# Kernel optimization log

Measured on AMD Instinct MI355X. Metric: run time of the kernel, lower is better.

## Reference

```python
import jax, jax.numpy as jnp
import numpy as np
from jax import lax

# SLAYER neuron / simulation constants (from netParams)
THETA = 10.0       # spike threshold
TAU_SR = 10.0      # synaptic (PSP) time constant
TAU_REF = 1.0      # refractory time constant
SCALE_REF = 2.0    # refractory scale
TAU_RHO = 1.0      # surrogate-gradient width (unused in fwd)
K_PSP = 32         # truncation length of SRM alpha kernel
K_REF = 16         # truncation length of refractory kernel

_t = np.arange(K_PSP, dtype=np.float64)
PSP_KERN = jnp.asarray((_t / TAU_SR) * np.exp(1.0 - _t / TAU_SR), jnp.float32)  # [K_PSP]
_tr = np.arange(1, K_REF + 1, dtype=np.float64)
REF_KERN = jnp.asarray(-SCALE_REF * THETA * (_tr / TAU_REF) * np.exp(1.0 - _tr / TAU_REF), jnp.float32)  # [K_REF]


def psp(x):
    """Causal temporal FIR filter with SRM alpha kernel; x: [..., T]."""
    sh = x.shape
    T = sh[-1]
    flat = x.reshape(-1, 1, T)                       # [B*, 1, T]
    k = PSP_KERN[::-1][None, None, :]                # correlation kernel (reversed)
    y = lax.conv_general_dilated(flat, k, (1,), [(K_PSP - 1, 0)])
    return y.reshape(sh)


def spike(u):
    """Threshold with refractory feedback, sequential over time. u: [..., T]."""
    uT = jnp.moveaxis(u, -1, 0)                      # [T, ...]
    buf0 = jnp.zeros(u.shape[:-1] + (K_REF,), u.dtype)

    def step(buf, ut):
        v = ut + buf[..., 0]
        s = (v >= THETA).astype(u.dtype)
        buf = jnp.concatenate([buf[..., 1:], jnp.zeros_like(buf[..., :1])], -1)
        buf = buf + s[..., None] * REF_KERN
        return buf, s

    _, sT = lax.scan(step, buf0, uT)
    return jnp.moveaxis(sT, 0, -1)


def conv_t(x, w, stride, pad):
    """2D conv applied independently per timestep. x: [N,C,H,W,T], w: [Co,C,kh,kw]."""
    N, C, H, W, T = x.shape
    xt = jnp.moveaxis(x, -1, 1).reshape(N * T, C, H, W)
    y = lax.conv_general_dilated(xt, w, (stride, stride), [(pad, pad), (pad, pad)])
    Co, Ho, Wo = y.shape[1], y.shape[2], y.shape[3]
    return jnp.moveaxis(y.reshape(N, T, Co, Ho, Wo), 1, -1)


def pool_t(x):
    """SLAYER sum-pool 2x2/s2 with weight 1.1*theta/kernel_area. x: [N,C,H,W,T]."""
    s = lax.reduce_window(x, np.float32(0.0), lax.add, (1, 1, 2, 2, 1), (1, 1, 2, 2, 1), 'VALID')
    return s * np.float32(1.1 * THETA / 4.0)


def setup_inputs() -> dict:
    key = jax.random.key(0)
    ks = jax.random.split(key, 5)
    spikeInput = (jax.random.uniform(ks[0], (4, 2, 256, 256, 50)) < 0.02).astype(jnp.float32)
    w1 = jax.random.normal(ks[1], (8, 2, 5, 5), jnp.float32) * 2.0
    w2 = jax.random.normal(ks[2], (16, 8, 3, 3), jnp.float32) * 1.5
    w3 = jax.random.normal(ks[3], (32, 16, 3, 3), jnp.float32) * 1.5
    w_fc = jax.random.normal(ks[4], (2, 32, 8, 8), jnp.float32) * 0.3
    return {"spikeInput": spikeInput, "w1": w1, "w2": w2, "w3": w3, "w_fc": w_fc}


def reference(spikeInput, w1, w2, w3, w_fc):
    x = spike(conv_t(psp(spikeInput), w1, 2, 1))   # [4,8,127,127,50]
    x = spike(pool_t(psp(x)))                      # [4,8,63,63,50]
    x = spike(conv_t(psp(x), w2, 2, 1))            # [4,16,32,32,50]
    x = spike(pool_t(psp(x)))                      # [4,16,16,16,50]
    x = spike(conv_t(psp(x), w3, 2, 1))            # [4,32,8,8,50]
    u = psp(x)
    out = jnp.einsum('ochw,nchwt->not', w_fc, u)   # dense over (C,H,W)
    return spike(out[:, :, None, None, :])         # [4,2,1,1,50]
```

## Files before the change

### kernel.cpp

```cpp
#include <hip/hip_runtime.h>
#include <cmath>

struct K32 { float k[32]; };
struct K16 { float k[16]; };

#define THETA 10.0f

__global__ __launch_bounds__(128)
void psp_kernel(const float* __restrict__ in, float* __restrict__ out,
                int nrows, K32 pk) {
  __shared__ __align__(16) float lds[64 * 50];
  const int rowBase = blockIdx.x * 64;
  const int tid = threadIdx.x;
  const int vr = min(64, nrows - rowBase);
  const int n4 = (vr * 50) >> 2;
  const float4* g4 = (const float4*)(in + (size_t)rowBase * 50);
  for (int i = tid; i < n4; i += 128) *(float4*)(&lds[4 * i]) = g4[i];
  __syncthreads();
  const int r = tid & 63;
  const int part = tid >> 6;
  const bool act = r < vr;
  float x[50];
  if (act) {
    if (part == 0) {
#pragma unroll
      for (int t = 0; t < 32; ++t) x[t] = lds[r * 50 + t];
    } else {
#pragma unroll
      for (int t = 0; t < 50; ++t) x[t] = lds[r * 50 + t];
    }
  }
  __syncthreads();
  if (act) {
    if (part == 0) {
#pragma unroll
      for (int t = 0; t < 32; ++t) {
        float a = 0.f;
#pragma unroll
        for (int k = 31; k >= 0; --k)
          if (t - k >= 0) a += x[t - k] * pk.k[k];
        lds[r * 50 + t] = a;
      }
    } else {
#pragma unroll
      for (int t = 32; t < 50; ++t) {
        float a = 0.f;
#pragma unroll
        for (int k = 31; k >= 0; --k)
          a += x[t - k] * pk.k[k];
        lds[r * 50 + t] = a;
      }
    }
  }
  __syncthreads();
  float4* o4 = (float4*)(out + (size_t)rowBase * 50);
  for (int i = tid; i < n4; i += 128) o4[i] = *(const float4*)(&lds[4 * i]);
}

template <int CIN, int COUT, int KK, int HIN, int WIN, int S1H, int S1W,
          int S2H, int S2W>
__global__ __launch_bounds__(256)
void conv_pps_kernel(const float* __restrict__ x, const float* __restrict__ w,
                     float* __restrict__ s2out, K32 pk, K16 rk) {
  constexpr int WT = 4;
  constexpr int SW = 8;
  constexpr int XR = 2 * (WT - 1) + KK;
  constexpr int GROUPS = (S1W + SW - 1) / SW;
  constexpr int NROW = COUT * 2 * SW;
  __shared__ float lds[NROW * 51];
  const int tid = threadIdx.x;
  const int wave = tid >> 6;
  const int lane = tid & 63;
  const int group = blockIdx.x % GROUPS;
  const int rest = blockIdx.x / GROUPS;
  const int hop = rest % S2H;
  const int n = rest / S2H;
  const int ho_off = wave & 1;
  const int wo_half = wave >> 1;
  const int ho = 2 * hop + ho_off;
  const int wo0 = group * SW + wo_half * WT;
  const int tt = lane < 50 ? lane : 49;

  float acc[COUT][WT] = {};
  for (int c = 0; c < CIN; ++c) {
#pragma unroll
    for (int kh = 0; kh < KK; ++kh) {
      const int hi = 2 * ho + kh - 1;
      if ((unsigned)hi >= (unsigned)HIN) continue;
      float xr[XR];
#pragma unroll
      for (int i = 0; i < XR; ++i) {
        const int wi = 2 * wo0 - 1 + i;
        xr[i] = ((unsigned)wi < (unsigned)WIN)
                    ? x[(((size_t)(n * CIN + c) * HIN + hi) * WIN + wi) * 50 + tt]
                    : 0.f;
      }
#pragma unroll
      for (int co = 0; co < COUT; ++co)
#pragma unroll
        for (int kw = 0; kw < KK; ++kw) {
          const float wv = w[((co * CIN + c) * KK + kh) * KK + kw];
#pragma unroll
          for (int wl = 0; wl < WT; ++wl)
            acc[co][wl] += xr[2 * wl + kw] * wv;
        }
    }
  }
  if (lane < 50) {
#pragma unroll
    for (int co = 0; co < COUT; ++co)
#pragma unroll
      for (int wl = 0; wl < WT; ++wl)
        lds[((co * 2 + ho_off) * SW + wo_half * WT + wl) * 51 + lane] = acc[co][wl];
  }
  __syncthreads();
  {
    const int r = tid & (NROW - 1);
    const int part = tid >> 7;
    const int wol = r & (SW - 1);
    const bool act = (group * SW + wol) < S1W;
    float xs[50];
    if (act) {
      if (part == 0) {
#pragma unroll
        for (int t = 0; t < 32; ++t) xs[t] = lds[r * 51 + t];
      } else {
#pragma unroll
        for (int t = 0; t < 50; ++t) xs[t] = lds[r * 51 + t];
      }
    }
    __syncthreads();
    if (act) {
      if (part == 0) {
        float buf[16];
#pragma unroll
        for (int j = 0; j < 16; ++j) buf[j] = 0.f;
#pragma unroll
        for (int t = 0; t < 32; ++t) {
          float v = xs[t] + buf[t & 15];
          buf[t & 15] = 0.f;
          float sp = 0.f;
          if (v >= THETA) {
            sp = 1.f;
#pragma unroll
            for (int j = 0; j < 16; ++j) buf[(t + 1 + j) & 15] += rk.k[j];
          }
          xs[t] = sp;
        }
#pragma unroll
        for (int t = 0; t < 32; ++t) {
          float a = 0.f;
#pragma unroll
          for (int k = 31; k >= 0; --k)
            if (t - k >= 0) a += xs[t - k] * pk.k[k];
          lds[r * 51 + t] = a;
        }
      } else {
        float buf[16];
#pragma unroll
        for (int j = 0; j < 16; ++j) buf[j] = 0.f;
#pragma unroll
        for (int t = 0; t < 50; ++t) {
          float v = xs[t] + buf[t & 15];
          buf[t & 15] = 0.f;
          float sp = 0.f;
          if (v >= THETA) {
            sp = 1.f;
#pragma unroll
            for (int j = 0; j < 16; ++j) buf[(t + 1 + j) & 15] += rk.k[j];
          }
          xs[t] = sp;
        }
#pragma unroll
        for (int t = 32; t < 50; ++t) {
          float a = 0.f;
#pragma unroll
          for (int k = 31; k >= 0; --k)
            a += xs[t - k] * pk.k[k];
          lds[r * 51 + t] = a;
        }
      }
    }
  }
  __syncthreads();
  if (tid < COUT * (SW / 2)) {
    const int co = tid / (SW / 2);
    const int wpl = tid % (SW / 2);
    const int wop = group * (SW / 2) + wpl;
    if (wop < S2W) {
      const int r00 = (co * 16 + 2 * wpl) * 51;
      const int r01 = (co * 16 + 2 * wpl + 1) * 51;
      const int r10 = (co * 16 + 8 + 2 * wpl) * 51;
      const int r11 = (co * 16 + 8 + 2 * wpl + 1) * 51;
      float* orow = s2out + (((size_t)(n * COUT + co) * S2H + hop) * S2W + wop) * 50;
      float buf[16];
#pragma unroll
      for (int j = 0; j < 16; ++j) buf[j] = 0.f;
      float prev = 0.f;
#pragma unroll
      for (int t = 0; t < 50; ++t) {
        const float u0 = (((lds[r00 + t] + lds[r01 + t]) + lds[r10 + t]) + lds[r11 + t]) * 2.75f;
        float v = u0 + buf[t & 15];
        buf[t & 15] = 0.f;
        float sp = 0.f;
        if (v >= THETA) {
          sp = 1.f;
#pragma unroll
          for (int j = 0; j < 16; ++j) buf[(t + 1 + j) & 15] += rk.k[j];
        }
        if (t & 1) *(float2*)(orow + t - 1) = make_float2(prev, sp);
        else prev = sp;
      }
    }
  }
}

template <int CIN, int COUT, int KK, int WT, int HIN, int WIN, int HOUT, int WOUT>
__global__ __launch_bounds__(256)
void conv_fir_spike_kernel(const float* __restrict__ x, const float* __restrict__ w,
                           float* __restrict__ s, K32 pk, K16 rk) {
  constexpr int XR = 2 * (WT - 1) + KK;
  constexpr int TW = 4 * WT;
  constexpr int GROUPS = (WOUT + TW - 1) / TW;
  constexpr int NROW = COUT * TW;
  __shared__ float lds[NROW * 51];
  const int tid = threadIdx.x;
  const int wave = tid >> 6;
  const int lane = tid & 63;
  const int group = blockIdx.x % GROUPS;
  const int rest = blockIdx.x / GROUPS;
  const int ho = rest % HOUT;
  const int n = rest / HOUT;
  const int wo0 = group * TW + wave * WT;
  const int tt = lane < 50 ? lane : 49;

  float acc[COUT][WT] = {};
  for (int c = 0; c < CIN; ++c) {
#pragma unroll
    for (int kh = 0; kh < KK; ++kh) {
      const int hi = 2 * ho + kh - 1;
      if ((unsigned)hi >= (unsigned)HIN) continue;
      float xr[XR];
#pragma unroll
      for (int i = 0; i < XR; ++i) {
        const int wi = 2 * wo0 - 1 + i;
        xr[i] = ((unsigned)wi < (unsigned)WIN)
                    ? x[(((size_t)(n * CIN + c) * HIN + hi) * WIN + wi) * 50 + tt]
                    : 0.f;
      }
#pragma unroll
      for (int co = 0; co < COUT; ++co)
#pragma unroll
        for (int kw = 0; kw < KK; ++kw) {
          const float wv = w[((co * CIN + c) * KK + kh) * KK + kw];
#pragma unroll
          for (int wl = 0; wl < WT; ++wl)
            acc[co][wl] += xr[2 * wl + kw] * wv;
        }
    }
  }

  if (lane < 50) {
#pragma unroll
    for (int co = 0; co < COUT; ++co)
#pragma unroll
      for (int wl = 0; wl < WT; ++wl)
        lds[(co * TW + wave * WT + wl) * 51 + lane] = acc[co][wl];
  }
  __syncthreads();
  {
    const int r = tid % NROW;
    const int part = tid / NROW;
    const int wol = r % TW;
    const bool act = (part < 2) && (group * TW + wol < WOUT);
    float xs[50];
    if (act) {
      if (part == 0) {
#pragma unroll
        for (int t = 0; t < 25; ++t) xs[t] = lds[r * 51 + t];
      } else {
#pragma unroll
        for (int t = 0; t < 50; ++t) xs[t] = lds[r * 51 + t];
      }
    }
    __syncthreads();
    if (act) {
      if (part == 0) {
#pragma unroll
        for (int t = 0; t < 25; ++t) {
          float a = 0.f;
#pragma unroll
          for (int k = 31; k >= 0; --k)
            if (t - k >= 0) a += xs[t - k] * pk.k[k];
          lds[r * 51 + t] = a;
        }
      } else {
#pragma unroll
        for (int t = 25; t < 50; ++t) {
          float a = 0.f;
#pragma unroll
          for (int k = 31; k >= 0; --k)
            if (t - k >= 0) a += xs[t - k] * pk.k[k];
          lds[r * 51 + t] = a;
        }
      }
    }
  }
  __syncthreads();
  if (tid < NROW) {
    const int co = tid / TW;
    const int wol = tid - co * TW;
    const int wo = group * TW + wol;
    if (wo < WOUT) {
      float* orow = s + (((size_t)(n * COUT + co) * HOUT + ho) * WOUT + wo) * 50;
      float buf[16];
#pragma unroll
      for (int j = 0; j < 16; ++j) buf[j] = 0.f;
      float prev = 0.f;
#pragma unroll
      for (int t = 0; t < 50; ++t) {
        float v = lds[tid * 51 + t] + buf[t & 15];
        buf[t & 15] = 0.f;
        float sp = 0.f;
        if (v >= THETA) {
          sp = 1.f;
#pragma unroll
          for (int j = 0; j < 16; ++j) buf[(t + 1 + j) & 15] += rk.k[j];
        }
        if (t & 1) *(float2*)(orow + t - 1) = make_float2(prev, sp);
        else prev = sp;
      }
    }
  }
}

__global__ __launch_bounds__(128)
void pool_fir_spike_kernel(const float* __restrict__ in, float* __restrict__ out,
                           int Hin, int Win, int Hout, int Wout, K32 pk, K16 rk) {
  __shared__ __align__(16) float lds[64 * 50 + 16 * 50];
  const int tid = threadIdx.x;
  const int ho = blockIdx.x % Hout;
  const int nc = blockIdx.x / Hout;
  const float* b0 = in + ((size_t)(nc * Hin + 2 * ho) * Win) * 50;
  const int n4 = (2 * Win * 50) >> 2;
  const float4* g4 = (const float4*)b0;
  for (int i = tid; i < n4; i += 128) *(float4*)(&lds[4 * i]) = g4[i];
  __syncthreads();
  {
    const int r = tid & 15;
    const int part = tid >> 4;
    const bool act = (part < 2) && (r < Wout);
    const int c00 = (2 * r) * 50, c01 = c00 + 50;
    const int c10 = Win * 50 + c00, c11 = Win * 50 + c01;
    const int ro = 64 * 50 + r * 50;
    float xs[50];
    if (act) {
      if (part == 0) {
#pragma unroll
        for (int t = 0; t < 25; ++t)
          xs[t] = (((lds[c00 + t] + lds[c01 + t]) + lds[c10 + t]) + lds[c11 + t]) * 2.75f;
#pragma unroll
        for (int t = 0; t < 25; ++t) {
          float a = 0.f;
#pragma unroll
          for (int k = 31; k >= 0; --k)
            if (t - k >= 0) a += xs[t - k] * pk.k[k];
          lds[ro + t] = a;
        }
      } else {
#pragma unroll
        for (int t = 0; t < 50; ++t)
          xs[t] = (((lds[c00 + t] + lds[c01 + t]) + lds[c10 + t]) + lds[c11 + t]) * 2.75f;
#pragma unroll
        for (int t = 25; t < 50; ++t) {
          float a = 0.f;
#pragma unroll
          for (int k = 31; k >= 0; --k)
            if (t - k >= 0) a += xs[t - k] * pk.k[k];
          lds[ro + t] = a;
        }
      }
    }
  }
  __syncthreads();
  if (tid < 16 && tid < Wout) {
    const int ro = 64 * 50 + tid * 50;
    float* orow = out + (((size_t)nc * Hout + ho) * Wout + tid) * 50;
    float buf[16];
#pragma unroll
    for (int j = 0; j < 16; ++j) buf[j] = 0.f;
    float prev = 0.f;
#pragma unroll
    for (int t = 0; t < 50; ++t) {
      float v = lds[ro + t] + buf[t & 15];
      buf[t & 15] = 0.f;
      float sp = 0.f;
      if (v >= THETA) {
        sp = 1.f;
#pragma unroll
        for (int j = 0; j < 16; ++j) buf[(t + 1 + j) & 15] += rk.k[j];
      }
      if (t & 1) *(float2*)(orow + t - 1) = make_float2(prev, sp);
      else prev = sp;
    }
  }
}

__global__ __launch_bounds__(512)
void fc_fir_spike_kernel(const float* __restrict__ w, const float* __restrict__ s,
                         float* __restrict__ out, K32 pk, K16 rk) {
  __shared__ float lds[8 * 51];
  const int tid = threadIdx.x;
  const int wave = tid >> 6, lane = tid & 63;
  const int o = wave & 1, n = wave >> 1;
  const int tt = lane < 50 ? lane : 49;
  const float* wrow = w + (size_t)o * 2048;
  const float* ub = s + (size_t)n * 2048 * 50;
  float acc = 0.f;
#pragma unroll 32
  for (int i = 0; i < 2048; ++i) acc += wrow[i] * ub[(size_t)i * 50 + tt];
  if (lane < 50) lds[wave * 51 + lane] = acc;
  __syncthreads();
  {
    const int r = tid & 7;
    const int part = tid >> 3;
    const bool act = part < 2;
    float xs[50];
    if (act) {
      if (part == 0) {
#pragma unroll
        for (int t = 0; t < 25; ++t) xs[t] = lds[r * 51 + t];
      } else {
#pragma unroll
        for (int t = 0; t < 50; ++t) xs[t] = lds[r * 51 + t];
      }
    }
    __syncthreads();
    if (act) {
      if (part == 0) {
#pragma unroll
        for (int t = 0; t < 25; ++t) {
          float a = 0.f;
#pragma unroll
          for (int k = 31; k >= 0; --k)
            if (t - k >= 0) a += xs[t - k] * pk.k[k];
          lds[r * 51 + t] = a;
        }
      } else {
#pragma unroll
        for (int t = 25; t < 50; ++t) {
          float a = 0.f;
#pragma unroll
          for (int k = 31; k >= 0; --k)
            if (t - k >= 0) a += xs[t - k] * pk.k[k];
          lds[r * 51 + t] = a;
        }
      }
    }
  }
  __syncthreads();
  if (tid < 8) {
    float buf[16];
#pragma unroll
    for (int j = 0; j < 16; ++j) buf[j] = 0.f;
#pragma unroll
    for (int t = 0; t < 50; ++t) {
      float v = lds[tid * 51 + t] + buf[t & 15];
      buf[t & 15] = 0.f;
      float sp = 0.f;
      if (v >= THETA) {
        sp = 1.f;
#pragma unroll
        for (int j = 0; j < 16; ++j) buf[(t + 1 + j) & 15] += rk.k[j];
      }
      out[tid * 50 + t] = sp;
    }
  }
}

extern "C" void kernel_launch(void* const* d_in, const int* in_sizes, int n_in,
                              void* d_out, int out_size, void* d_ws, size_t ws_size,
                              hipStream_t stream) {
  const float* xin = (const float*)d_in[0];
  const float* w1  = (const float*)d_in[1];
  const float* w2  = (const float*)d_in[2];
  const float* w3  = (const float*)d_in[3];
  const float* wfc = (const float*)d_in[4];
  float* out = (float*)d_out;

  float* R0 = (float*)d_ws;
  float* R1 = R0 + 26214400;

  K32 pk;
  for (int k = 0; k < 32; ++k)
    pk.k[k] = (float)(((double)k / 10.0) * exp(1.0 - (double)k / 10.0));
  K16 rk;
  for (int j = 0; j < 16; ++j) {
    const double tr = (double)(j + 1);
    rk.k[j] = (float)(-2.0 * 10.0 * tr * exp(1.0 - tr));
  }

  psp_kernel<<<8192, 128, 0, stream>>>(xin, R0, 524288, pk);
  conv_pps_kernel<2, 8, 5, 256, 256, 127, 127, 63, 63>
      <<<4 * 63 * 16, 256, 0, stream>>>(R0, w1, R1, pk, rk);
  conv_fir_spike_kernel<8, 16, 3, 1, 63, 63, 32, 32>
      <<<4 * 32 * 8, 256, 0, stream>>>(R1, w2, R0, pk, rk);
  pool_fir_spike_kernel<<<4 * 16 * 16, 128, 0, stream>>>(R0, R1, 32, 32, 16, 16, pk, rk);
  conv_fir_spike_kernel<16, 32, 3, 1, 16, 16, 8, 8>
      <<<4 * 8 * 2, 256, 0, stream>>>(R1, w3, R0, pk, rk);
  fc_fir_spike_kernel<<<1, 512, 0, stream>>>(wfc, R0, out, pk, rk);
}
```

Before: 482.7 us.

## Fuse second conv stage with pool, PSP and spike into one kernel

Adds a kernel that computes conv2 for a 2x4 output tile, applies PSP filtering and refractory spiking in LDS, then does 2x2 sum-pooling, a second PSP and a second spike before writing the pooled output. This replaces the separate conv_fir_spike and pool_fir_spike launches. It removes one launch and the global write and read of the unpooled spike tensor. In exchange each block carries more serial work and there are fewer blocks, which may hurt latency hiding.

```diff
diff --git a/kernel.cpp b/kernel.cpp
--- a/kernel.cpp
+++ b/kernel.cpp
@@ -215,6 +215,187 @@
   }
 }
 
+template <int CIN, int COUT, int KK, int SW, int WT, int HIN, int WIN,
+          int S1H, int S1W, int S2H, int S2W>
+__global__ __launch_bounds__(256)
+void conv_pps2_kernel(const float* __restrict__ x, const float* __restrict__ w,
+                      float* __restrict__ s2out, K32 pk, K16 rk) {
+  constexpr int XR = 2 * (WT - 1) + KK;
+  constexpr int GROUPS = (S1W + SW - 1) / SW;
+  constexpr int NROW = COUT * 2 * SW;
+  constexpr int NROWP = COUT * (SW / 2);
+  __shared__ float lds[NROW * 51];
+  const int tid = threadIdx.x;
+  const int wave = tid >> 6;
+  const int lane = tid & 63;
+  const int group = blockIdx.x % GROUPS;
+  const int rest = blockIdx.x / GROUPS;
+  const int hop = rest % S2H;
+  const int n = rest / S2H;
+  const int ho_off = wave & 1;
+  const int wo_half = wave >> 1;
+  const int ho = 2 * hop + ho_off;
+  const int wo0 = group * SW + wo_half * WT;
+  const int tt = lane < 50 ? lane : 49;
+
+  float acc[COUT][WT] = {};
+  for (int c = 0; c < CIN; ++c) {
+#pragma unroll
+    for (int kh = 0; kh < KK; ++kh) {
+      const int hi = 2 * ho + kh - 1;
+      if ((unsigned)hi >= (unsigned)HIN) continue;
+      float xr[XR];
+#pragma unroll
+      for (int i = 0; i < XR; ++i) {
+        const int wi = 2 * wo0 - 1 + i;
+        xr[i] = ((unsigned)wi < (unsigned)WIN)
+                    ? x[(((size_t)(n * CIN + c) * HIN + hi) * WIN + wi) * 50 + tt]
+                    : 0.f;
+      }
+#pragma unroll
+      for (int co = 0; co < COUT; ++co)
+#pragma unroll
+        for (int kw = 0; kw < KK; ++kw) {
+          const float wv = w[((co * CIN + c) * KK + kh) * KK + kw];
+#pragma unroll
+          for (int wl = 0; wl < WT; ++wl)
+            acc[co][wl] += xr[2 * wl + kw] * wv;
+        }
+    }
+  }
+  if (lane < 50) {
+#pragma unroll
+    for (int co = 0; co < COUT; ++co)
+#pragma unroll
+      for (int wl = 0; wl < WT; ++wl)
+        lds[((co * 2 + ho_off) * SW + wo_half * WT + wl) * 51 + lane] = acc[co][wl];
+  }
+  __syncthreads();
+  {
+    const int r = tid & (NROW - 1);
+    const int part = tid >> 7;
+    float xs[50];
+    if (part == 0) {
+#pragma unroll
+      for (int t = 0; t < 32; ++t) xs[t] = lds[r * 51 + t];
+    } else {
+#pragma unroll
+      for (int t = 0; t < 50; ++t) xs[t] = lds[r * 51 + t];
+    }
+    __syncthreads();
+    if (part == 0) {
+#pragma unroll
+      for (int t = 0; t < 32; ++t) {
+        float a = 0.f;
+#pragma unroll
+        for (int k = 31; k >= 0; --k)
+          if (t - k >= 0) a += xs[t - k] * pk.k[k];
+        lds[r * 51 + t] = a;
+      }
+    } else {
+#pragma unroll
+      for (int t = 32; t < 50; ++t) {
+        float a = 0.f;
+#pragma unroll
+        for (int k = 31; k >= 0; --k)
+          a += xs[t - k] * pk.k[k];
+        lds[r * 51 + t] = a;
+      }
+    }
+  }
+  __syncthreads();
+  if (tid < NROW) {
+    float buf[16];
+#pragma unroll
+    for (int j = 0; j < 16; ++j) buf[j] = 0.f;
+#pragma unroll
+    for (int t = 0; t < 50; ++t) {
+      float v = lds[tid * 51 + t] + buf[t & 15];
+      buf[t & 15] = 0.f;
+      float sp = 0.f;
+      if (v >= THETA) {
+        sp = 1.f;
+#pragma unroll
+        for (int j = 0; j < 16; ++j) buf[(t + 1 + j) & 15] += rk.k[j];
+      }
+      lds[tid * 51 + t] = sp;
+    }
+  }
+  __syncthreads();
+  {
+    const int r = tid & (NROWP - 1);
+    const int part = tid >> 5;
+    const bool act = part < 2;
+    const int co = r / (SW / 2);
+    const int wpl = r % (SW / 2);
+    const int r00 = ((co * 2) * SW + 2 * wpl) * 51;
+    const int r01 = r00 + 51;
+    const int r10 = ((co * 2 + 1) * SW + 2 * wpl) * 51;
+    const int r11 = r10 + 51;
+    float xs[50];
+    if (act) {
+      if (part == 0) {
+#pragma unroll
+        for (int t = 0; t < 32; ++t)
+          xs[t] = (((lds[r00 + t] + lds[r01 + t]) + lds[r10 + t]) + lds[r11 + t]) * 2.75f;
+      } else {
+#pragma unroll
+        for (int t = 0; t < 50; ++t)
+          xs[t] = (((lds[r00 + t] + lds[r01 + t]) + lds[r10 + t]) + lds[r11 + t]) * 2.75f;
+      }
+    }
+    __syncthreads();
+    if (act) {
+      if (part == 0) {
+#pragma unroll
+        for (int t = 0; t < 32; ++t) {
+          float a = 0.f;
+#pragma unroll
+          for (int k = 31; k >= 0; --k)
+            if (t - k >= 0) a += xs[t - k] * pk.k[k];
+          lds[r00 + t] = a;
+        }
+      } else {
+#pragma unroll
+        for (int t = 32; t < 50; ++t) {
+          float a = 0.f;
+#pragma unroll
+          for (int k = 31; k >= 0; --k)
+            a += xs[t - k] * pk.k[k];
+          lds[r00 + t] = a;
+        }
+      }
+    }
+  }
+  __syncthreads();
+  if (tid < NROWP) {
+    const int co = tid / (SW / 2);
+    const int wpl = tid % (SW / 2);
+    const int wop = group * (SW / 2) + wpl;
+    if (wop < S2W) {
+      const int r00 = ((co * 2) * SW + 2 * wpl) * 51;
+      float* orow = s2out + (((size_t)(n * COUT + co) * S2H + hop) * S2W + wop) * 50;
+      float buf[16];
+#pragma unroll
+      for (int j = 0; j < 16; ++j) buf[j] = 0.f;
+      float prev = 0.f;
+#pragma unroll
+      for (int t = 0; t < 50; ++t) {
+        float v = lds[r00 + t] + buf[t & 15];
+        buf[t & 15] = 0.f;
+        float sp = 0.f;
+        if (v >= THETA) {
+          sp = 1.f;
+#pragma unroll
+          for (int j = 0; j < 16; ++j) buf[(t + 1 + j) & 15] += rk.k[j];
+        }
+        if (t & 1) *(float2*)(orow + t - 1) = make_float2(prev, sp);
+        else prev = sp;
+      }
+    }
+  }
+}
+
 template <int CIN, int COUT, int KK, int WT, int HIN, int WIN, int HOUT, int WOUT>
 __global__ __launch_bounds__(256)
 void conv_fir_spike_kernel(const float* __restrict__ x, const float* __restrict__ w,
@@ -334,78 +515,6 @@
   }
 }
 
-__global__ __launch_bounds__(128)
-void pool_fir_spike_kernel(const float* __restrict__ in, float* __restrict__ out,
-                           int Hin, int Win, int Hout, int Wout, K32 pk, K16 rk) {
-  __shared__ __align__(16) float lds[64 * 50 + 16 * 50];
-  const int tid = threadIdx.x;
-  const int ho = blockIdx.x % Hout;
-  const int nc = blockIdx.x / Hout;
-  const float* b0 = in + ((size_t)(nc * Hin + 2 * ho) * Win) * 50;
-  const int n4 = (2 * Win * 50) >> 2;
-  const float4* g4 = (const float4*)b0;
-  for (int i = tid; i < n4; i += 128) *(float4*)(&lds[4 * i]) = g4[i];
-  __syncthreads();
-  {
-    const int r = tid & 15;
-    const int part = tid >> 4;
-    const bool act = (part < 2) && (r < Wout);
-    const int c00 = (2 * r) * 50, c01 = c00 + 50;
-    const int c10 = Win * 50 + c00, c11 = Win * 50 + c01;
-    const int ro = 64 * 50 + r * 50;
-    float xs[50];
-    if (act) {
-      if (part == 0) {
-#pragma unroll
-        for (int t = 0; t < 25; ++t)
-          xs[t] = (((lds[c00 + t] + lds[c01 + t]) + lds[c10 + t]) + lds[c11 + t]) * 2.75f;
-#pragma unroll
-        for (int t = 0; t < 25; ++t) {
-          float a = 0.f;
-#pragma unroll
-          for (int k = 31; k >= 0; --k)
-            if (t - k >= 0) a += xs[t - k] * pk.k[k];
-          lds[ro + t] = a;
-        }
-      } else {
-#pragma unroll
-        for (int t = 0; t < 50; ++t)
-          xs[t] = (((lds[c00 + t] + lds[c01 + t]) + lds[c10 + t]) + lds[c11 + t]) * 2.75f;
-#pragma unroll
-        for (int t = 25; t < 50; ++t) {
-          float a = 0.f;
-#pragma unroll
-          for (int k = 31; k >= 0; --k)
-            if (t - k >= 0) a += xs[t - k] * pk.k[k];
-          lds[ro + t] = a;
-        }
-      }
-    }
-  }
-  __syncthreads();
-  if (tid < 16 && tid < Wout) {
-    const int ro = 64 * 50 + tid * 50;
-    float* orow = out + (((size_t)nc * Hout + ho) * Wout + tid) * 50;
-    float buf[16];
-#pragma unroll
-    for (int j = 0; j < 16; ++j) buf[j] = 0.f;
-    float prev = 0.f;
-#pragma unroll
-    for (int t = 0; t < 50; ++t) {
-      float v = lds[ro + t] + buf[t & 15];
-      buf[t & 15] = 0.f;
-      float sp = 0.f;
-      if (v >= THETA) {
-        sp = 1.f;
-#pragma unroll
-        for (int j = 0; j < 16; ++j) buf[(t + 1 + j) & 15] += rk.k[j];
-      }
-      if (t & 1) *(float2*)(orow + t - 1) = make_float2(prev, sp);
-      else prev = sp;
-    }
-  }
-}
-
 __global__ __launch_bounds__(512)
 void fc_fir_spike_kernel(const float* __restrict__ w, const float* __restrict__ s,
                          float* __restrict__ out, K32 pk, K16 rk) {
@@ -503,10 +612,9 @@
   psp_kernel<<<8192, 128, 0, stream>>>(xin, R0, 524288, pk);
   conv_pps_kernel<2, 8, 5, 256, 256, 127, 127, 63, 63>
       <<<4 * 63 * 16, 256, 0, stream>>>(R0, w1, R1, pk, rk);
-  conv_fir_spike_kernel<8, 16, 3, 1, 63, 63, 32, 32>
-      <<<4 * 32 * 8, 256, 0, stream>>>(R1, w2, R0, pk, rk);
-  pool_fir_spike_kernel<<<4 * 16 * 16, 128, 0, stream>>>(R0, R1, 32, 32, 16, 16, pk, rk);
+  conv_pps2_kernel<8, 16, 3, 4, 2, 63, 63, 32, 32, 16, 16>
+      <<<4 * 16 * 8, 256, 0, stream>>>(R1, w2, R0, pk, rk);
   conv_fir_spike_kernel<16, 32, 3, 1, 16, 16, 8, 8>
-      <<<4 * 8 * 2, 256, 0, stream>>>(R1, w3, R0, pk, rk);
-  fc_fir_spike_kernel<<<1, 512, 0, stream>>>(wfc, R0, out, pk, rk);
+      <<<4 * 8 * 2, 256, 0, stream>>>(R0, w3, R1, pk, rk);
+  fc_fir_spike_kernel<<<1, 512, 0, stream>>>(wfc, R1, out, pk, rk);
 }
```

New measurement: 479.3 us. No clear change (-0.7%).
